# Optimization experiments

Measured on AMD Instinct MI355X. Metric: run time of the kernel, lower is better.

The kernel has to match this reference:

```python
import jax, jax.numpy as jnp
import numpy as np

# Hyperparameters matching init_kwargs
IN_CH = 64
OUT_CH = 128
KERNEL = (3, 3)
STRIDE = (1, 1)
PADDING = 'SAME'
K_ORDER = 3          # spline order
G_INTERVALS = 3      # grid intervals
GRID_MIN, GRID_MAX = -1.0, 1.0
N_BASIS = G_INTERVALS + K_ORDER  # basis functions per input = 6
PATCH_DIM = IN_CH * KERNEL[0] * KERNEL[1]  # 576


def _grid():
    # Extended uniform knot vector: G + 2k + 1 knots
    h = (GRID_MAX - GRID_MIN) / G_INTERVALS
    return jnp.arange(-K_ORDER, G_INTERVALS + K_ORDER + 1, dtype=jnp.float32) * h + GRID_MIN


def _b_splines(x):
    # x: [N, n_in] -> bases: [N, n_in, G + k]
    grid = _grid()  # [G + 2k + 1]
    xe = x[..., None]  # [N, n_in, 1]
    bases = ((xe >= grid[:-1]) & (xe < grid[1:])).astype(x.dtype)  # order-0, [N, n_in, G+2k]
    for p in range(1, K_ORDER + 1):
        left = (xe - grid[: -(p + 1)]) / (grid[p:-1] - grid[: -(p + 1)]) * bases[..., :-1]
        right = (grid[p + 1:] - xe) / (grid[p + 1:] - grid[1:-p]) * bases[..., 1:]
        bases = left + right
    return bases  # [N, n_in, G + k]


def setup_inputs() -> dict:
    key = jax.random.key(0)
    k0, k1, k2, k3 = jax.random.split(key, 4)
    x = jax.random.normal(k0, (8, 64, 64, IN_CH), dtype=jnp.float32)
    base_w = jax.random.normal(k1, (OUT_CH, PATCH_DIM), dtype=jnp.float32) * 0.05
    spline_w = jax.random.normal(k2, (OUT_CH, PATCH_DIM, N_BASIS), dtype=jnp.float32) * 0.05
    bias = jax.random.normal(k3, (OUT_CH,), dtype=jnp.float32) * 0.05
    return {'x': x, 'base_w': base_w, 'spline_w': spline_w, 'bias': bias}


def reference(x, base_w, spline_w, bias):
    batch = x.shape[0]
    dn = ('NHWC', 'HWIO', 'NHWC')
    patches = jax.lax.conv_general_dilated_patches(
        lhs=x, filter_shape=KERNEL, window_strides=STRIDE, padding=PADDING,
        dimension_numbers=dn)  # [B, H, W, patch_dim]
    out_spatial = patches.shape[1:-1]
    p = patches.reshape(-1, PATCH_DIM)  # [N, patch_dim]
    # EfficientKAN: residual (silu) branch + spline branch + bias
    base_out = jax.nn.silu(p) @ base_w.T                      # [N, out]
    bases = _b_splines(p)                                      # [N, patch_dim, G+k]
    spline_out = jnp.einsum('nig,oig->no', bases, spline_w)    # [N, out]
    y = base_out + spline_out + bias
    return y.reshape(batch, *out_spatial, OUT_CH)
```

## Files before the change

kernel.cpp:

```cpp
#include <hip/hip_runtime.h>

typedef __attribute__((ext_vector_type(8))) short short8;
typedef __attribute__((ext_vector_type(16))) float f32x16;

#define FT2_SHORTS (512u * 4356u * 8u)
#define PLANE16    4356

typedef __attribute__((address_space(3))) unsigned int lds_u32_t;
typedef __attribute__((address_space(1))) const unsigned int g_u32_t;

__device__ __forceinline__ unsigned short f2bf(float x) {
    union { float f; unsigned u; } v; v.f = x;
    unsigned r = v.u + 0x7FFFu + ((v.u >> 16) & 1u);
    return (unsigned short)(r >> 16);
}

__device__ __forceinline__ void feat8(float p, unsigned short* uf) {
    float e   = __expf(-p);
    float sig = 1.f / (1.f + e);
    uf[0] = f2bf(p * sig);
    float u  = p * 1.5f + 4.5f;
    float fj = floorf(u);
    int   j0 = (int)fj;
    float t  = u - fj;
    bool  inr = (u >= 0.f) && (u < 9.f);
    float t2 = t * t, t3 = t2 * t;
    const float c16 = 1.f / 6.f;
    float r0 = t3 * c16;
    float r1 = (-3.f * t3 + 3.f * t2 + 3.f * t + 1.f) * c16;
    float r2 = (3.f * t3 - 6.f * t2 + 4.f) * c16;
    float s1 = 1.f - t;
    float r3 = s1 * s1 * s1 * c16;
#pragma unroll
    for (int g = 0; g < 6; ++g) {
        int r = j0 - g;
        float v = (r == 0) ? r0 : ((r == 1) ? r1 : ((r == 2) ? r2 : ((r == 3) ? r3 : 0.f)));
        uf[1 + g] = f2bf(inr ? v : 0.f);
    }
    uf[7] = 0;
}

__global__ __launch_bounds__(256)
void prep_all(const float* __restrict__ x,
              const float* __restrict__ bw, const float* __restrict__ sw,
              unsigned short* __restrict__ ft, unsigned short* __restrict__ wt) {
    const int blk  = blockIdx.x;
    const int tid  = threadIdx.x;
    const int line = blk >> 2;
    const int q    = blk & 3;

    if (tid < 36) {
        int idx = blk * 36 + tid;
        int o = idx / 576;
        int i = idx - o * 576;
        int slab = i >> 3, e = i & 7;
        union { unsigned short u[8]; uint4 v; } pk;
        pk.u[0] = f2bf(bw[o * 576 + i]);
        const float* s = sw + (size_t)(o * 576 + i) * 6;
#pragma unroll
        for (int f = 0; f < 6; ++f) pk.u[1 + f] = f2bf(s[f]);
        pk.u[7] = 0;
        *(uint4*)(wt + ((size_t)slab * 8192 + e * 1024 + o * 8)) = pk.v;
    }

    if (tid < 65) {
        int t = q * 65 + tid;
        short8 pad = { 0, 0, (short)0x3CAB, (short)0x3EF5,
                       (short)0x3EF5, (short)0x3CAB, 0, 0 };
        int yy, xx;
        if (t < 66)       { yy = 0;       xx = t; }
        else if (t < 132) { yy = 65;      xx = t - 66; }
        else if (t < 196) { yy = t - 131; xx = 0; }
        else              { yy = t - 195; xx = 65; }
        ((short8*)ft)[line * PLANE16 + yy * 66 + xx] = pad;
    }

    const int xx = tid & 63;
    const int cw = tid >> 6;
    const int b  = line >> 6, y = line & 63;
    const int c0 = q * 16 + cw * 4;
    const float4 v = *(const float4*)(x + (size_t)line * 4096 + xx * 64 + c0);

    union { unsigned short u[8]; uint4 w; } p0, p1, p2, p3;
    feat8(v.x, p0.u); feat8(v.y, p1.u); feat8(v.z, p2.u); feat8(v.w, p3.u);

    const size_t cell = (size_t)(y + 1) * 66 + (xx + 1);
    *(uint4*)(ft + ((((size_t)((c0 + 0) * 8 + b) * PLANE16) + cell) << 3)) = p0.w;
    *(uint4*)(ft + ((((size_t)((c0 + 1) * 8 + b) * PLANE16) + cell) << 3)) = p1.w;
    *(uint4*)(ft + ((((size_t)((c0 + 2) * 8 + b) * PLANE16) + cell) << 3)) = p2.w;
    *(uint4*)(ft + ((((size_t)((c0 + 3) * 8 + b) * PLANE16) + cell) << 3)) = p3.w;
}

#define BUF_SHORTS 12288

#define STAGE(sl, q_)                                                                 \
    {                                                                                 \
        unsigned short* bufq = Bufs + (q_) * BUF_SHORTS;                              \
        const unsigned short* bsrc = wt + (size_t)(sl) * 8192;                        \
        _Pragma("unroll")                                                             \
        for (int t = 0; t < 3; ++t) {                                                 \
            int u = wave * 3 + t;                     \
            if (u < 16) {                                                             \
                int boff = u * 512 + lane * 8;                                        \
                __builtin_amdgcn_global_load_lds((g_u32_t*)(bsrc + boff),             \
                                                 (lds_u32_t*)(bufq + boff), 16, 0, 0);\
            } else {                                                                  \
                int idx = u - 16;                                     \
                int ia  = (sl) * 8 + idx;                                             \
                int c_  = (ia * 7282) >> 16;                                          \
                int i9_ = ia - c_ * 9;                                                \
                int kh_ = (i9_ * 11) >> 5;                                            \
                int kw_ = i9_ - kh_ * 3;                                              \
                const unsigned short* asrc = ft +                                     \
                    (((size_t)(c_ * 8 + b) * PLANE16 + (y + kh_) * 66 + kw_) << 3)    \
                    + lane * 8;                                                       \
                unsigned short* adst = bufq + 8192 + idx * 512 + lane * 8;            \
                __builtin_amdgcn_global_load_lds((g_u32_t*)asrc, (lds_u32_t*)adst,    \
                                                 16, 0, 0);                           \
            }                                                                         \
        }                                                                             \
    }

#define COMPUTE(q_)                                                                   \
    {                                                                                 \
        const unsigned short* bufr = Bufs + (q_) * BUF_SHORTS;                        \
        const unsigned short* Ab = bufr + 8192 + iloc * 512;                          \
        const unsigned short* Bb = bufr + iloc * 1024 + nh * 512;                     \
        short8 a0 = *(const short8*)(Ab + l32 * 8);                                   \
        short8 a1 = *(const short8*)(Ab + (32 + l32) * 8);                            \
        short8 b0 = *(const short8*)(Bb + l32 * 8);                                   \
        short8 b1 = *(const short8*)(Bb + 256 + l32 * 8);                             \
        acc00 = __builtin_amdgcn_mfma_f32_32x32x16_bf16(a0, b0, acc00, 0, 0, 0);      \
        acc01 = __builtin_amdgcn_mfma_f32_32x32x16_bf16(a0, b1, acc01, 0, 0, 0);      \
        acc10 = __builtin_amdgcn_mfma_f32_32x32x16_bf16(a1, b0, acc10, 0, 0, 0);      \
        acc11 = __builtin_amdgcn_mfma_f32_32x32x16_bf16(a1, b1, acc11, 0, 0, 0);      \
    }

#define PHASE(q_, n_, stagesl, dostage_)                                              \
    {                                                                                 \
        asm volatile("s_waitcnt vmcnt(" #n_ ")" ::: "memory");                        \
        __builtin_amdgcn_s_barrier();                                                 \
        asm volatile("" ::: "memory");                                                \
        __builtin_amdgcn_s_setprio(1);                                                \
        COMPUTE(q_)                                                                   \
        __builtin_amdgcn_s_setprio(0);                                                \
        asm volatile("" ::: "memory");                                                \
        __builtin_amdgcn_s_barrier();                                                 \
        asm volatile("" ::: "memory");                                                \
        if (dostage_) STAGE(stagesl, q_);                                             \
    }

#define DUMPA(base_, A_)                                                              \
    {   float4* s4 = (float4*)(red + (base_));                                        \
        _Pragma("unroll")                                                             \
        for (int c = 0; c < 4; ++c)                                                   \
            s4[c * 64 + lane] = make_float4(A_[4*c], A_[4*c+1], A_[4*c+2], A_[4*c+3]); }
#define ADDA(base_, A_)                                                               \
    {   const float4* s4 = (const float4*)(red + (base_));                            \
        _Pragma("unroll")                                                             \
        for (int c = 0; c < 4; ++c) {                                                 \
            float4 rv = s4[c * 64 + lane];                                            \
            A_[4*c] += rv.x; A_[4*c+1] += rv.y; A_[4*c+2] += rv.z; A_[4*c+3] += rv.w; } }

__global__ __launch_bounds__(512, 4)
void convkan_gemm(const unsigned short* __restrict__ ft,
                  const unsigned short* __restrict__ wt,
                  const float* __restrict__ bias,
                  float* __restrict__ out) {
    extern __shared__ unsigned short Bufs[];

    const int tid  = threadIdx.x;
    const int blk  = blockIdx.x;
    const int mb   = ((blk & 7) << 6) | (blk >> 3);
    const int lane = tid & 63;
    const int wave = tid >> 6;
    const int kq   = wave >> 1;
    const int nh   = wave & 1;
    const int l32  = lane & 31;
    const int h    = lane >> 5;
    const int iloc = (kq << 1) + h;

    const int b = mb >> 6;
    const int y = mb & 63;

    f32x16 acc00, acc01, acc10, acc11;
#pragma unroll
    for (int e = 0; e < 16; ++e) { acc00[e] = 0.f; acc01[e] = 0.f; acc10[e] = 0.f; acc11[e] = 0.f; }

    STAGE(0, 0);
    STAGE(1, 1);
    STAGE(2, 2);

    for (int it3 = 0; it3 < 23; ++it3) {
        const int it = it3 * 3;
        PHASE(0, 6, it + 3, true)
        PHASE(1, 6, it + 4, true)
        PHASE(2, 6, it + 5, true)
    }
    PHASE(0, 6, 0, false)
    PHASE(1, 3, 0, false)
    PHASE(2, 0, 0, false)

    __syncthreads();
    float* red = (float*)Bufs;

    if (kq >= 2) { DUMPA(((nh << 1) + (kq - 2)) * 2048,        acc00);
                   DUMPA(((nh << 1) + (kq - 2)) * 2048 + 1024, acc01); }
    __syncthreads();
    if (kq < 2)  { ADDA(((nh << 1) + kq) * 2048,        acc00);
                   ADDA(((nh << 1) + kq) * 2048 + 1024, acc01); }
    __syncthreads();
    if (kq >= 2) { DUMPA(((nh << 1) + (kq - 2)) * 2048,        acc10);
                   DUMPA(((nh << 1) + (kq - 2)) * 2048 + 1024, acc11); }
    __syncthreads();
    if (kq < 2)  { ADDA(((nh << 1) + kq) * 2048,        acc10);
                   ADDA(((nh << 1) + kq) * 2048 + 1024, acc11); }
    __syncthreads();
    if (kq == 1) { DUMPA(nh * 4096,        acc00); DUMPA(nh * 4096 + 1024, acc01);
                   DUMPA(nh * 4096 + 2048, acc10); DUMPA(nh * 4096 + 3072, acc11); }
    __syncthreads();
    if (kq == 0) {
        ADDA(nh * 4096,        acc00); ADDA(nh * 4096 + 1024, acc01);
        ADDA(nh * 4096 + 2048, acc10); ADDA(nh * 4096 + 3072, acc11);

        const int ncol = nh * 64 + l32;
        const float bv0 = bias[ncol];
        const float bv1 = bias[ncol + 32];
        const int prow = mb * 64;
#pragma unroll
        for (int r = 0; r < 16; ++r) {
            int mrow = (r & 3) + ((r >> 2) << 3) + 4 * h;
            float* p = out + (size_t)(prow + mrow) * 128 + ncol;
            p[0]  = acc00[r] + bv0;
            p[32] = acc01[r] + bv1;
            float* p2 = out + (size_t)(prow + 32 + mrow) * 128 + ncol;
            p2[0]  = acc10[r] + bv0;
            p2[32] = acc11[r] + bv1;
        }
    }
}

extern "C" void kernel_launch(void* const* d_in, const int* in_sizes, int n_in,
                              void* d_out, int out_size, void* d_ws, size_t ws_size,
                              hipStream_t stream) {
    (void)in_sizes; (void)n_in; (void)ws_size; (void)out_size;
    const float* x        = (const float*)d_in[0];
    const float* base_w   = (const float*)d_in[1];
    const float* spline_w = (const float*)d_in[2];
    const float* bias     = (const float*)d_in[3];
    float* out = (float*)d_out;

    unsigned short* ft = (unsigned short*)d_ws;
    unsigned short* wt = ft + FT2_SHORTS;

    hipLaunchKernelGGL(prep_all, dim3(2048), dim3(256), 0, stream,
                       x, base_w, spline_w, ft, wt);

    const int shmem = 3 * BUF_SHORTS * 2;
    (void)hipFuncSetAttribute((const void*)convkan_gemm,
                              hipFuncAttributeMaxDynamicSharedMemorySize, shmem);
    hipLaunchKernelGGL(convkan_gemm, dim3(512), dim3(512), shmem, stream,
                       ft, wt, bias, out);
}
```

Before: 129.9 us.

## Repack features channel-innermost per basis to drop zero-padded eighth feature slot

```diff
diff --git a/kernel.cpp b/kernel.cpp
--- a/kernel.cpp
+++ b/kernel.cpp
@@ -3,8 +3,8 @@
 typedef __attribute__((ext_vector_type(8))) short short8;
 typedef __attribute__((ext_vector_type(16))) float f32x16;
 
-#define FT2_SHORTS (512u * 4356u * 8u)
-#define PLANE16    4356
+#define FT3_SHORTS 15611904u
+#define PLANE_FB   278784u
 
 typedef __attribute__((address_space(3))) unsigned int lds_u32_t;
 typedef __attribute__((address_space(1))) const unsigned int g_u32_t;
@@ -15,7 +15,7 @@
     return (unsigned short)(r >> 16);
 }
 
-__device__ __forceinline__ void feat8(float p, unsigned short* uf) {
+__device__ __forceinline__ void feat7(float p, unsigned short* uf) {
     float e   = __expf(-p);
     float sig = 1.f / (1.f + e);
     uf[0] = f2bf(p * sig);
@@ -37,7 +37,6 @@
         float v = (r == 0) ? r0 : ((r == 1) ? r1 : ((r == 2) ? r2 : ((r == 3) ? r3 : 0.f)));
         uf[1 + g] = f2bf(inr ? v : 0.f);
     }
-    uf[7] = 0;
 }
 
 __global__ __launch_bounds__(256)
@@ -46,49 +45,66 @@
               unsigned short* __restrict__ ft, unsigned short* __restrict__ wt) {
     const int blk  = blockIdx.x;
     const int tid  = threadIdx.x;
-    const int line = blk >> 2;
-    const int q    = blk & 3;
-
-    if (tid < 36) {
-        int idx = blk * 36 + tid;
+    const int line = blk >> 1;
+    const int half = blk & 1;
+
+    if (tid < 72) {
+        int idx = blk * 72 + tid;
         int o = idx / 576;
         int i = idx - o * 576;
-        int slab = i >> 3, e = i & 7;
-        union { unsigned short u[8]; uint4 v; } pk;
-        pk.u[0] = f2bf(bw[o * 576 + i]);
-        const float* s = sw + (size_t)(o * 576 + i) * 6;
-#pragma unroll
-        for (int f = 0; f < 6; ++f) pk.u[1 + f] = f2bf(s[f]);
-        pk.u[7] = 0;
-        *(uint4*)(wt + ((size_t)slab * 8192 + e * 1024 + o * 8)) = pk.v;
-    }
-
-    if (tid < 65) {
-        int t = q * 65 + tid;
-        short8 pad = { 0, 0, (short)0x3CAB, (short)0x3EF5,
-                       (short)0x3EF5, (short)0x3CAB, 0, 0 };
-        int yy, xx;
-        if (t < 66)       { yy = 0;       xx = t; }
-        else if (t < 132) { yy = 65;      xx = t - 66; }
-        else if (t < 196) { yy = t - 131; xx = 0; }
-        else              { yy = t - 195; xx = 65; }
-        ((short8*)ft)[line * PLANE16 + yy * 66 + xx] = pad;
-    }
-
-    const int xx = tid & 63;
-    const int cw = tid >> 6;
-    const int b  = line >> 6, y = line & 63;
-    const int c0 = q * 16 + cw * 4;
-    const float4 v = *(const float4*)(x + (size_t)line * 4096 + xx * 64 + c0);
-
-    union { unsigned short u[8]; uint4 w; } p0, p1, p2, p3;
-    feat8(v.x, p0.u); feat8(v.y, p1.u); feat8(v.z, p2.u); feat8(v.w, p3.u);
-
-    const size_t cell = (size_t)(y + 1) * 66 + (xx + 1);
-    *(uint4*)(ft + ((((size_t)((c0 + 0) * 8 + b) * PLANE16) + cell) << 3)) = p0.w;
-    *(uint4*)(ft + ((((size_t)((c0 + 1) * 8 + b) * PLANE16) + cell) << 3)) = p1.w;
-    *(uint4*)(ft + ((((size_t)((c0 + 2) * 8 + b) * PLANE16) + cell) << 3)) = p2.w;
-    *(uint4*)(ft + ((((size_t)((c0 + 3) * 8 + b) * PLANE16) + cell) << 3)) = p3.w;
+        int c = i / 9;
+        int j = i - c * 9;
+        int e = c >> 4, hh = (c >> 3) & 1, slot = c & 7;
+        size_t base = (size_t)(e * 2 + hh) * 1024 + o * 8 + slot;
+        const float* s6 = sw + (size_t)(o * 576 + i) * 6;
+        wt[(size_t)j * 8192 + base] = f2bf(bw[o * 576 + i]);
+#pragma unroll
+        for (int f = 1; f < 7; ++f)
+            wt[(size_t)(f * 9 + j) * 8192 + base] = f2bf(s6[f - 1]);
+    }
+
+    {
+        int t = blk * 114 + tid;
+        if (tid < 114 && t < 116480) {
+            int cell = t % 260;
+            int rem  = t / 260;
+            int chb_ = rem & 7, b_ = (rem >> 3) & 7, f_ = rem >> 6;
+            const unsigned short padv[7] =
+                { 0, 0, 0x3CAB, 0x3EF5, 0x3EF5, 0x3CAB, 0 };
+            unsigned short pv = padv[f_];
+            int yy, xx;
+            if (cell < 66)       { yy = 0;          xx = cell; }
+            else if (cell < 132) { yy = 65;         xx = cell - 66; }
+            else if (cell < 196) { yy = cell - 131; xx = 0; }
+            else                 { yy = cell - 195; xx = 65; }
+            union { unsigned short u[8]; uint4 v; } pk;
+#pragma unroll
+            for (int k = 0; k < 8; ++k) pk.u[k] = pv;
+            size_t off = ((((size_t)(f_ * 8 + b_) * 66 + yy) * 8 + chb_) * 66 + xx) * 8;
+            *(uint4*)(ft + off) = pk.v;
+        }
+    }
+
+    const int xx  = tid & 63;
+    const int g   = tid >> 6;
+    const int chb = half * 4 + g;
+    const int b   = line >> 6, y = line & 63;
+
+    float4 v0 = *(const float4*)(x + (size_t)line * 4096 + xx * 64 + chb * 8);
+    float4 v1 = *(const float4*)(x + (size_t)line * 4096 + xx * 64 + chb * 8 + 4);
+
+    unsigned short uf[8][7];
+    feat7(v0.x, uf[0]); feat7(v0.y, uf[1]); feat7(v0.z, uf[2]); feat7(v0.w, uf[3]);
+    feat7(v1.x, uf[4]); feat7(v1.y, uf[5]); feat7(v1.z, uf[6]); feat7(v1.w, uf[7]);
+
+#pragma unroll
+    for (int f = 0; f < 7; ++f) {
+        union { unsigned short u[8]; uint4 w; } pk;
+#pragma unroll
+        for (int ch = 0; ch < 8; ++ch) pk.u[ch] = uf[ch][f];
+        size_t off = ((((size_t)(f * 8 + b) * 66 + (y + 1)) * 8 + chb) * 66 + (xx + 1)) * 8;
+        *(uint4*)(ft + off) = pk.w;
+    }
 }
 
 #define BUF_SHORTS 12288
@@ -96,7 +112,13 @@
 #define STAGE(sl, q_)                                                                 \
     {                                                                                 \
         unsigned short* bufq = Bufs + (q_) * BUF_SHORTS;                              \
+        int f_  = ((sl) * 7282) >> 16;                                                \
+        int j_  = (sl) - f_ * 9;                                                      \
+        int kh_ = (j_ * 11) >> 5;                                                     \
+        int kw_ = j_ - kh_ * 3;                                                       \
         const unsigned short* bsrc = wt + (size_t)(sl) * 8192;                        \
+        const unsigned short* abase = ft +                                            \
+            ((((size_t)(f_ * 8 + b) * 66 + (y + kh_)) * 8) * 66 + kw_) * 8;           \
         _Pragma("unroll")                                                             \
         for (int t = 0; t < 3; ++t) {                                                 \
             int u = wave * 3 + t;                     \
@@ -105,16 +127,9 @@
                 __builtin_amdgcn_global_load_lds((g_u32_t*)(bsrc + boff),             \
                                                  (lds_u32_t*)(bufq + boff), 16, 0, 0);\
             } else {                                                                  \
-                int idx = u - 16;                                     \
-                int ia  = (sl) * 8 + idx;                                             \
-                int c_  = (ia * 7282) >> 16;                                          \
-                int i9_ = ia - c_ * 9;                                                \
-                int kh_ = (i9_ * 11) >> 5;                                            \
-                int kw_ = i9_ - kh_ * 3;                                              \
-                const unsigned short* asrc = ft +                                     \
-                    (((size_t)(c_ * 8 + b) * PLANE16 + (y + kh_) * 66 + kw_) << 3)    \
-                    + lane * 8;                                                       \
-                unsigned short* adst = bufq + 8192 + idx * 512 + lane * 8;            \
+                int chb = u - 16;                                           \
+                const unsigned short* asrc = abase + chb * 528 + lane * 8;            \
+                unsigned short* adst = bufq + 8192 + chb * 512 + lane * 8;            \
                 __builtin_amdgcn_global_load_lds((g_u32_t*)asrc, (lds_u32_t*)adst,    \
                                                  16, 0, 0);                           \
             }                                                                         \
@@ -191,7 +206,7 @@
     STAGE(1, 1);
     STAGE(2, 2);
 
-    for (int it3 = 0; it3 < 23; ++it3) {
+    for (int it3 = 0; it3 < 20; ++it3) {
         const int it = it3 * 3;
         PHASE(0, 6, it + 3, true)
         PHASE(1, 6, it + 4, true)
@@ -251,9 +266,9 @@
     float* out = (float*)d_out;
 
     unsigned short* ft = (unsigned short*)d_ws;
-    unsigned short* wt = ft + FT2_SHORTS;
-
-    hipLaunchKernelGGL(prep_all, dim3(2048), dim3(256), 0, stream,
+    unsigned short* wt = ft + FT3_SHORTS;
+
+    hipLaunchKernelGGL(prep_all, dim3(1024), dim3(256), 0, stream,
                        x, base_w, spline_w, ft, wt);
 
     const int shmem = 3 * BUF_SHORTS * 2;
```

Result: slower. 136.6 us (+5.1%).

## Use 128-row tiles with split-K across two blocks and atomic accumulation

Applied to the files above, without the earlier changes.

```diff
diff --git a/kernel.cpp b/kernel.cpp
--- a/kernel.cpp
+++ b/kernel.cpp
@@ -91,30 +91,31 @@
     *(uint4*)(ft + ((((size_t)((c0 + 3) * 8 + b) * PLANE16) + cell) << 3)) = p3.w;
 }
 
-#define BUF_SHORTS 12288
+#define BUF_SHORTS 16384
 
 #define STAGE(sl, q_)                                                                 \
     {                                                                                 \
         unsigned short* bufq = Bufs + (q_) * BUF_SHORTS;                              \
         const unsigned short* bsrc = wt + (size_t)(sl) * 8192;                        \
         _Pragma("unroll")                                                             \
-        for (int t = 0; t < 3; ++t) {                                                 \
-            int u = wave * 3 + t;                     \
+        for (int t = 0; t < 4; ++t) {                                                 \
+            int u = wave * 4 + t;                     \
             if (u < 16) {                                                             \
                 int boff = u * 512 + lane * 8;                                        \
                 __builtin_amdgcn_global_load_lds((g_u32_t*)(bsrc + boff),             \
                                                  (lds_u32_t*)(bufq + boff), 16, 0, 0);\
             } else {                                                                  \
-                int idx = u - 16;                                     \
-                int ia  = (sl) * 8 + idx;                                             \
+                int ua  = u - 16;                          \
+                int ia  = (sl) * 8 + (ua >> 1);                                       \
+                int ln  = ua & 1;                                                     \
                 int c_  = (ia * 7282) >> 16;                                          \
                 int i9_ = ia - c_ * 9;                                                \
                 int kh_ = (i9_ * 11) >> 5;                                            \
                 int kw_ = i9_ - kh_ * 3;                                              \
                 const unsigned short* asrc = ft +                                     \
-                    (((size_t)(c_ * 8 + b) * PLANE16 + (y + kh_) * 66 + kw_) << 3)    \
-                    + lane * 8;                                                       \
-                unsigned short* adst = bufq + 8192 + idx * 512 + lane * 8;            \
+                    (((size_t)(c_ * 8 + b) * PLANE16 + (y0 + ln + kh_) * 66 + kw_)    \
+                     << 3) + lane * 8;                                                \
+                unsigned short* adst = bufq + 8192 + ua * 512 + lane * 8;             \
                 __builtin_amdgcn_global_load_lds((g_u32_t*)asrc, (lds_u32_t*)adst,    \
                                                  16, 0, 0);                           \
             }                                                                         \
@@ -124,12 +125,19 @@
 #define COMPUTE(q_)                                                                   \
     {                                                                                 \
         const unsigned short* bufr = Bufs + (q_) * BUF_SHORTS;                        \
-        const unsigned short* Ab = bufr + 8192 + iloc * 512;                          \
-        const unsigned short* Bb = bufr + iloc * 1024 + nh * 512;                     \
-        short8 a0 = *(const short8*)(Ab + l32 * 8);                                   \
-        short8 a1 = *(const short8*)(Ab + (32 + l32) * 8);                            \
-        short8 b0 = *(const short8*)(Bb + l32 * 8);                                   \
-        short8 b1 = *(const short8*)(Bb + 256 + l32 * 8);                             \
+        short8 a0, a1, b0, b1;                                                        \
+        a0 = *(const short8*)(bufr + ao0);                                            \
+        a1 = *(const short8*)(bufr + ao0 + 256);                                      \
+        b0 = *(const short8*)(bufr + bo0);                                            \
+        b1 = *(const short8*)(bufr + bo0 + 256);                                      \
+        acc00 = __builtin_amdgcn_mfma_f32_32x32x16_bf16(a0, b0, acc00, 0, 0, 0);      \
+        acc01 = __builtin_amdgcn_mfma_f32_32x32x16_bf16(a0, b1, acc01, 0, 0, 0);      \
+        acc10 = __builtin_amdgcn_mfma_f32_32x32x16_bf16(a1, b0, acc10, 0, 0, 0);      \
+        acc11 = __builtin_amdgcn_mfma_f32_32x32x16_bf16(a1, b1, acc11, 0, 0, 0);      \
+        a0 = *(const short8*)(bufr + ao1);                                            \
+        a1 = *(const short8*)(bufr + ao1 + 256);                                      \
+        b0 = *(const short8*)(bufr + bo1);                                            \
+        b1 = *(const short8*)(bufr + bo1 + 256);                                      \
         acc00 = __builtin_amdgcn_mfma_f32_32x32x16_bf16(a0, b0, acc00, 0, 0, 0);      \
         acc01 = __builtin_amdgcn_mfma_f32_32x32x16_bf16(a0, b1, acc01, 0, 0, 0);      \
         acc10 = __builtin_amdgcn_mfma_f32_32x32x16_bf16(a1, b0, acc10, 0, 0, 0);      \
@@ -171,71 +179,69 @@
 
     const int tid  = threadIdx.x;
     const int blk  = blockIdx.x;
-    const int mb   = ((blk & 7) << 6) | (blk >> 3);
+    const int kk   = blk >> 8;
+    const int mbr  = blk & 255;
+    const int mb   = ((mbr & 7) << 5) | (mbr >> 3);
     const int lane = tid & 63;
     const int wave = tid >> 6;
-    const int kq   = wave >> 1;
+    const int kq   = wave >> 2;
+    const int mh   = (wave >> 1) & 1;
     const int nh   = wave & 1;
     const int l32  = lane & 31;
     const int h    = lane >> 5;
-    const int iloc = (kq << 1) + h;
-
-    const int b = mb >> 6;
-    const int y = mb & 63;
+
+    const int b  = mb >> 5;
+    const int y0 = (mb & 31) << 1;
+    const int kk36 = kk * 36;
+
+    const int il0 = 4 * kq + h;
+    const int il1 = 4 * kq + 2 + h;
+    const int ao0 = 8192 + (il0 * 2 + mh) * 512 + l32 * 8;
+    const int ao1 = 8192 + (il1 * 2 + mh) * 512 + l32 * 8;
+    const int bo0 = il0 * 1024 + nh * 512 + l32 * 8;
+    const int bo1 = il1 * 1024 + nh * 512 + l32 * 8;
 
     f32x16 acc00, acc01, acc10, acc11;
 #pragma unroll
     for (int e = 0; e < 16; ++e) { acc00[e] = 0.f; acc01[e] = 0.f; acc10[e] = 0.f; acc11[e] = 0.f; }
 
-    STAGE(0, 0);
-    STAGE(1, 1);
-    STAGE(2, 2);
-
-    for (int it3 = 0; it3 < 23; ++it3) {
-        const int it = it3 * 3;
-        PHASE(0, 6, it + 3, true)
-        PHASE(1, 6, it + 4, true)
-        PHASE(2, 6, it + 5, true)
-    }
-    PHASE(0, 6, 0, false)
-    PHASE(1, 3, 0, false)
-    PHASE(2, 0, 0, false)
+    STAGE(kk36 + 0, 0);
+    STAGE(kk36 + 1, 1);
+
+    for (int it2 = 0; it2 < 17; ++it2) {
+        const int it = it2 * 2;
+        PHASE(0, 4, kk36 + it + 2, true)
+        PHASE(1, 4, kk36 + it + 3, true)
+    }
+    PHASE(0, 4, 0, false)
+    PHASE(1, 0, 0, false)
 
     __syncthreads();
     float* red = (float*)Bufs;
-
-    if (kq >= 2) { DUMPA(((nh << 1) + (kq - 2)) * 2048,        acc00);
-                   DUMPA(((nh << 1) + (kq - 2)) * 2048 + 1024, acc01); }
-    __syncthreads();
-    if (kq < 2)  { ADDA(((nh << 1) + kq) * 2048,        acc00);
-                   ADDA(((nh << 1) + kq) * 2048 + 1024, acc01); }
-    __syncthreads();
-    if (kq >= 2) { DUMPA(((nh << 1) + (kq - 2)) * 2048,        acc10);
-                   DUMPA(((nh << 1) + (kq - 2)) * 2048 + 1024, acc11); }
-    __syncthreads();
-    if (kq < 2)  { ADDA(((nh << 1) + kq) * 2048,        acc10);
-                   ADDA(((nh << 1) + kq) * 2048 + 1024, acc11); }
-    __syncthreads();
-    if (kq == 1) { DUMPA(nh * 4096,        acc00); DUMPA(nh * 4096 + 1024, acc01);
-                   DUMPA(nh * 4096 + 2048, acc10); DUMPA(nh * 4096 + 3072, acc11); }
+    const int grp = mh * 2 + nh;
+
+    if (kq == 1) {
+        DUMPA(grp * 4096,        acc00); DUMPA(grp * 4096 + 1024, acc01);
+        DUMPA(grp * 4096 + 2048, acc10); DUMPA(grp * 4096 + 3072, acc11);
+    }
     __syncthreads();
     if (kq == 0) {
-        ADDA(nh * 4096,        acc00); ADDA(nh * 4096 + 1024, acc01);
-        ADDA(nh * 4096 + 2048, acc10); ADDA(nh * 4096 + 3072, acc11);
+        ADDA(grp * 4096,        acc00); ADDA(grp * 4096 + 1024, acc01);
+        ADDA(grp * 4096 + 2048, acc10); ADDA(grp * 4096 + 3072, acc11);
 
         const int ncol = nh * 64 + l32;
-        const float bv0 = bias[ncol];
-        const float bv1 = bias[ncol + 32];
-        const int prow = mb * 64;
+        const float bv0 = kk ? 0.f : bias[ncol];
+        const float bv1 = kk ? 0.f : bias[ncol + 32];
+        const int prow = mb * 128 + mh * 64;
 #pragma unroll
         for (int r = 0; r < 16; ++r) {
             int mrow = (r & 3) + ((r >> 2) << 3) + 4 * h;
             float* p = out + (size_t)(prow + mrow) * 128 + ncol;
-            p[0]  = acc00[r] + bv0;
-            p[32] = acc01[r] + bv1;
+            atomicAdd(p,      acc00[r] + bv0);
+            atomicAdd(p + 32, acc01[r] + bv1);
             float* p2 = out + (size_t)(prow + 32 + mrow) * 128 + ncol;
-            p2[0]  = acc10[r] + bv0;
-            p2[32] = acc11[r] + bv1;
+            atomicAdd(p2,      acc10[r] + bv0);
+            atomicAdd(p2 + 32, acc11[r] + bv1);
         }
     }
 }
@@ -243,7 +249,7 @@
 extern "C" void kernel_launch(void* const* d_in, const int* in_sizes, int n_in,
                               void* d_out, int out_size, void* d_ws, size_t ws_size,
                               hipStream_t stream) {
-    (void)in_sizes; (void)n_in; (void)ws_size; (void)out_size;
+    (void)in_sizes; (void)n_in; (void)ws_size;
     const float* x        = (const float*)d_in[0];
     const float* base_w   = (const float*)d_in[1];
     const float* spline_w = (const float*)d_in[2];
@@ -253,10 +259,11 @@
     unsigned short* ft = (unsigned short*)d_ws;
     unsigned short* wt = ft + FT2_SHORTS;
 
+    hipMemsetAsync(out, 0, (size_t)out_size * sizeof(float), stream);
     hipLaunchKernelGGL(prep_all, dim3(2048), dim3(256), 0, stream,
                        x, base_w, spline_w, ft, wt);
 
-    const int shmem = 3 * BUF_SHORTS * 2;
+    const int shmem = 2 * BUF_SHORTS * 2;
     (void)hipFuncSetAttribute((const void*)convkan_gemm,
                               hipFuncAttributeMaxDynamicSharedMemorySize, shmem);
     hipLaunchKernelGGL(convkan_gemm, dim3(512), dim3(512), shmem, stream,
```

After: 237.3 us. 1.83x slower.
